# Optimization experiments

Hardware: AMD Instinct MI355X
Metric: run time of the kernel (lower is better)

## Reference

```python
import jax, jax.numpy as jnp
import numpy as np

STRIDE = 1
PADDING = 1
GROUPS = 1


def setup_inputs() -> dict:
    key = jax.random.key(0)
    kx, kw, kb = jax.random.split(key, 3)
    x_int = jax.random.randint(kx, (16, 256, 56, 56), 0, 127, dtype=jnp.int32)
    weight_int = jax.random.randint(kw, (256, 256, 3, 3), 0, 127, dtype=jnp.int32)
    bias_int = jax.random.randint(kb, (256,), 0, 127, dtype=jnp.int32)
    return {"x_int": x_int, "weight_int": weight_int, "bias_int": bias_int}


def reference(x_int, weight_int, bias_int):
    # Integer conv2d with int32 accumulation, exactly F.conv2d semantics.
    y = jax.lax.conv_general_dilated(
        x_int,
        weight_int,
        window_strides=(STRIDE, STRIDE),
        padding=((PADDING, PADDING), (PADDING, PADDING)),
        dimension_numbers=("NCHW", "OIHW", "NCHW"),
        feature_group_count=GROUPS,
    )
    # bias broadcast over [B, Cout, H, W]
    return y + bias_int[None, :, None, None]
```

## Files before the change

kernel.cpp:

```cpp
#include <hip/hip_runtime.h>


typedef int v4i  __attribute__((ext_vector_type(4)));
typedef int v16i __attribute__((ext_vector_type(16)));

#define X8_ROWSTRIDE 1856
#define X8_IMGSTRIDE 107648
#define X8_BYTES     13778944
#define W8_CHUNK     18432
#define XS_OFF       36864
#define XS_BUF       30720

typedef const __attribute__((address_space(1))) unsigned char* gptr_t;
typedef __attribute__((address_space(3))) unsigned char* lptr_t;

__device__ __forceinline__ int pack4(const int* p, int stride) {
  return (p[0] & 255) | ((p[stride] & 255) << 8) |
         ((p[2 * stride] & 255) << 16) | ((p[3 * stride] & 255) << 24);
}

__global__ __launch_bounds__(256)
void pack_all(const int* __restrict__ x, const int* __restrict__ wgt,
              unsigned char* __restrict__ ws8) {
  const int blk = blockIdx.x;
  if (blk < 784) {
    const int gid = blk * 256 + threadIdx.x;
    const int srcg = gid & 1;
    int t = gid >> 1;
    const int sq = t % 14;  t /= 14;
    const int row = t % 56 + 1;
    const int cb  = t / 56;
    const int chunk = cb >> 4, b = cb & 15;
    const int ci0 = chunk * 32 + srcg * 16;
    const int* src = x + (b * 256 + ci0) * 3136 + (row - 1) * 56 + 4 * sq;
    v4i L[16];
    #pragma unroll
    for (int ch = 0; ch < 16; ++ch) L[ch] = *(const v4i*)(src + ch * 3136);
    unsigned char* dstrow = ws8 + cb * X8_IMGSTRIDE + row * X8_ROWSTRIDE;
    #pragma unroll
    for (int j = 0; j < 4; ++j) {
      const int slot = 4 * sq + 1 + j;
      v4i g;
      #pragma unroll
      for (int d = 0; d < 4; ++d)
        g[d] = (L[4 * d][j] & 255) | ((L[4 * d + 1][j] & 255) << 8) |
               ((L[4 * d + 2][j] & 255) << 16) | ((L[4 * d + 3][j] & 255) << 24);
      const int p = (srcg + slot) & 1;
      *(v4i*)(dstrow + slot * 32 + p * 16) = g;
    }
  } else if (blk < 1012) {
    const int g2 = (blk - 784) * 256 + threadIdx.x;
    const int cb = g2 / 456;
    const int r  = g2 - cb * 456;
    int off;
    if (r < 232) {
      const int row = r < 116 ? 0 : 57;
      const int rr = r % 116;
      off = row * X8_ROWSTRIDE + (rr >> 1) * 32 + (rr & 1) * 16;
    } else {
      const int r2 = r - 232;
      const int row = (r2 >> 2) + 1;
      const int slot = (r2 & 2) ? 57 : 0;
      off = row * X8_ROWSTRIDE + slot * 32 + (r2 & 1) * 16;
    }
    *(v4i*)(ws8 + cb * X8_IMGSTRIDE + off) = (v4i){0, 0, 0, 0};
  } else {
    const int gw = (blk - 1012) * 256 + threadIdx.x;
    const int p = gw & 1;
    int t = gw >> 1;
    const int tap = t % 9;  t /= 9;
    const int co = t & 63;
    const int tcc = t >> 6;
    const int chunk = tcc & 7, cotile = tcc >> 3;
    const int srcg = (p + co) & 1;
    const int ci0 = chunk * 32 + srcg * 16;
    const int* src = wgt + ((cotile * 64 + co) * 256 + ci0) * 9 + tap;
    v4i v = (v4i){pack4(src, 9), pack4(src + 36, 9),
                  pack4(src + 72, 9), pack4(src + 108, 9)};
    *(v4i*)(ws8 + X8_BYTES + (t * 9 + tap) * 32 + p * 16) = v;
  }
}

__device__ __forceinline__ void stage_chunk(const unsigned char* wg,
                                            const unsigned char* xg,
                                            unsigned char* ldsb, int c, int tid) {
  const unsigned char* wsrc = wg + c * W8_CHUNK;
  unsigned char* wdst = ldsb + (c & 1) * W8_CHUNK;
  __builtin_amdgcn_global_load_lds((gptr_t)(wsrc + tid * 16),
                                   (lptr_t)(wdst + tid * 16), 16, 0, 0);
  __builtin_amdgcn_global_load_lds((gptr_t)(wsrc + 8192 + tid * 16),
                                   (lptr_t)(wdst + 8192 + tid * 16), 16, 0, 0);
  if (tid < 128)
    __builtin_amdgcn_global_load_lds((gptr_t)(wsrc + 16384 + tid * 16),
                                     (lptr_t)(wdst + 16384 + tid * 16), 16, 0, 0);
  const unsigned char* xsrc = xg + c * (16 * X8_IMGSTRIDE);
  unsigned char* xdst = ldsb + XS_OFF + (c & 1) * XS_BUF;
  #pragma unroll
  for (int i = 0; i < 3; ++i)
    __builtin_amdgcn_global_load_lds((gptr_t)(xsrc + i * 8192 + tid * 16),
                                     (lptr_t)(xdst + i * 8192 + tid * 16), 16, 0, 0);
  if (tid < 384)
    __builtin_amdgcn_global_load_lds((gptr_t)(xsrc + 24576 + tid * 16),
                                     (lptr_t)(xdst + 24576 + tid * 16), 16, 0, 0);
}

__global__ __launch_bounds__(512, 2)
void conv_main(const unsigned char* __restrict__ ws8, const int* __restrict__ bias,
               int* __restrict__ out) {
  __shared__ __align__(16) unsigned char lds[2 * W8_CHUNK + 2 * XS_BUF];
  __shared__ int bls[64];

  const int tid = threadIdx.x, lane = tid & 63, wv = tid >> 6;
  const int n = lane & 31, gq = lane >> 5;
  const int tc = blockIdx.y;
  const int hb = blockIdx.x;
  const int hg = hb >> 4, b = hb & 15;
  const int h0 = hg * 14;

  if (tid < 64) bls[tid] = bias[tc * 64 + tid];

  const int abase = n * 288 + (((gq + n) & 1) << 4);
  int boff[3][4];
  #pragma unroll
  for (int kw = 0; kw < 3; ++kw)
    #pragma unroll
    for (int bt = 0; bt < 4; ++bt) {
      int slot = bt * 16 + (n & 15) + kw;
      if (slot > 57) slot = 57;
      boff[kw][bt] = slot * 32 + (((gq + slot) & 1) << 4);
    }
  const int rbase = (2 * wv + (n >> 4)) * X8_ROWSTRIDE;

  v16i acc[2][4];
  #pragma unroll
  for (int i = 0; i < 2; ++i)
    #pragma unroll
    for (int j = 0; j < 4; ++j)
      acc[i][j] = (v16i){0,0,0,0,0,0,0,0,0,0,0,0,0,0,0,0};

  const unsigned char* wg = ws8 + X8_BYTES + tc * (8 * W8_CHUNK);
  const unsigned char* xg = ws8 + b * X8_IMGSTRIDE + h0 * X8_ROWSTRIDE;

  stage_chunk(wg, xg, lds, 0, tid);
  for (int c = 0; c < 8; ++c) {
    __syncthreads();
    if (c < 7) stage_chunk(wg, xg, lds, c + 1, tid);
    if (wv < 7) {
      const unsigned char* wls = lds + (c & 1) * W8_CHUNK;
      const unsigned char* xs  = lds + XS_OFF + (c & 1) * XS_BUF;
      #pragma unroll
      for (int kh = 0; kh < 3; ++kh) {
        const unsigned char* xr = xs + rbase + kh * X8_ROWSTRIDE;
        #pragma unroll
        for (int kw = 0; kw < 3; ++kw) {
          const int tap = kh * 3 + kw;
          const v4i a0 = *(const v4i*)(wls + abase + tap * 32);
          const v4i a1 = *(const v4i*)(wls + 9216 + abase + tap * 32);
          #pragma unroll
          for (int bt = 0; bt < 4; ++bt) {
            const v4i bb = *(const v4i*)(xr + boff[kw][bt]);
            acc[0][bt] = __builtin_amdgcn_mfma_i32_32x32x32_i8(a0, bb, acc[0][bt], 0, 0, 0);
            acc[1][bt] = __builtin_amdgcn_mfma_i32_32x32x32_i8(a1, bb, acc[1][bt], 0, 0, 0);
          }
        }
      }
    }
  }

  if (wv >= 7) return;
  const int h = h0 + 2 * wv + (n >> 4);
  const int wbase = lane & 15;
  #pragma unroll
  for (int ct = 0; ct < 2; ++ct) {
    #pragma unroll
    for (int r = 0; r < 16; ++r) {
      const int co64 = ct * 32 + (r & 3) + 8 * (r >> 2) + 4 * gq;
      const int bv = bls[co64];
      int* orow = out + ((b * 256 + tc * 64 + co64) * 56 + h) * 56;
      #pragma unroll
      for (int bt = 0; bt < 4; ++bt) {
        const int w0 = bt * 16 + wbase;
        if (w0 < 56) orow[w0] = acc[ct][bt][r] + bv;
      }
    }
  }
}

extern "C" void kernel_launch(void* const* d_in, const int* in_sizes, int n_in,
                              void* d_out, int out_size, void* d_ws, size_t ws_size,
                              hipStream_t stream) {
  const int* x    = (const int*)d_in[0];
  const int* w    = (const int*)d_in[1];
  const int* bias = (const int*)d_in[2];
  unsigned char* ws8 = (unsigned char*)d_ws;
  hipLaunchKernelGGL(pack_all, dim3(1156), dim3(256), 0, stream, x, w, ws8);
  hipLaunchKernelGGL(conv_main, dim3(64, 4, 1), dim3(512), 0, stream,
                     ws8, bias, (int*)d_out);
}
```

Measured before the change: 131.3 us.

## Triple-buffer LDS staging with vmcnt-gated barriers to prefetch two chunks ahead

Moves the weight and input staging in LDS from double to triple buffering, so chunk c+2 is prefetched while chunk c is computed. Each wait now uses s_waitcnt vmcnt(6) on only the older stage's async global-to-LDS loads, followed by a raw s_barrier, in place of a full __syncthreads. The per-thread load distribution is rebalanced so every thread issues exactly six loads per stage, which the vmcnt count relies on. The cost is LDS growing to about 147KB, which likely allows only one 512-thread block per CU. With a 256-block grid this may not reduce effective occupancy.

```diff
diff --git a/kernel.cpp b/kernel.cpp
--- a/kernel.cpp
+++ b/kernel.cpp
@@ -8,7 +8,7 @@
 #define X8_IMGSTRIDE 107648
 #define X8_BYTES     13778944
 #define W8_CHUNK     18432
-#define XS_OFF       36864
+#define XS_OFF       55296
 #define XS_BUF       30720
 
 typedef const __attribute__((address_space(1))) unsigned char* gptr_t;
@@ -83,31 +83,35 @@
 
 __device__ __forceinline__ void stage_chunk(const unsigned char* wg,
                                             const unsigned char* xg,
-                                            unsigned char* ldsb, int c, int tid) {
+                                            unsigned char* ldsb, int c, int buf,
+                                            int tid) {
   const unsigned char* wsrc = wg + c * W8_CHUNK;
-  unsigned char* wdst = ldsb + (c & 1) * W8_CHUNK;
-  __builtin_amdgcn_global_load_lds((gptr_t)(wsrc + tid * 16),
-                                   (lptr_t)(wdst + tid * 16), 16, 0, 0);
-  __builtin_amdgcn_global_load_lds((gptr_t)(wsrc + 8192 + tid * 16),
-                                   (lptr_t)(wdst + 8192 + tid * 16), 16, 0, 0);
-  if (tid < 128)
-    __builtin_amdgcn_global_load_lds((gptr_t)(wsrc + 16384 + tid * 16),
-                                     (lptr_t)(wdst + 16384 + tid * 16), 16, 0, 0);
   const unsigned char* xsrc = xg + c * (16 * X8_IMGSTRIDE);
-  unsigned char* xdst = ldsb + XS_OFF + (c & 1) * XS_BUF;
-  #pragma unroll
-  for (int i = 0; i < 3; ++i)
-    __builtin_amdgcn_global_load_lds((gptr_t)(xsrc + i * 8192 + tid * 16),
-                                     (lptr_t)(xdst + i * 8192 + tid * 16), 16, 0, 0);
-  if (tid < 384)
-    __builtin_amdgcn_global_load_lds((gptr_t)(xsrc + 24576 + tid * 16),
-                                     (lptr_t)(xdst + 24576 + tid * 16), 16, 0, 0);
+  unsigned char* wdst = ldsb + buf * W8_CHUNK;
+  unsigned char* xdst = ldsb + XS_OFF + buf * XS_BUF;
+  #pragma unroll
+  for (int i = 0; i < 2; ++i) {
+    const int o = (tid + i * 512) * 16;
+    __builtin_amdgcn_global_load_lds((gptr_t)(wsrc + o), (lptr_t)(wdst + o), 16, 0, 0);
+  }
+  if (tid < 128) {
+    const int o = (1024 + tid) * 16;
+    __builtin_amdgcn_global_load_lds((gptr_t)(wsrc + o), (lptr_t)(wdst + o), 16, 0, 0);
+  } else {
+    const int o = (tid - 128) * 16;
+    __builtin_amdgcn_global_load_lds((gptr_t)(xsrc + o), (lptr_t)(xdst + o), 16, 0, 0);
+  }
+  #pragma unroll
+  for (int i = 0; i < 3; ++i) {
+    const int o = (384 + tid + i * 512) * 16;
+    __builtin_amdgcn_global_load_lds((gptr_t)(xsrc + o), (lptr_t)(xdst + o), 16, 0, 0);
+  }
 }
 
 __global__ __launch_bounds__(512, 2)
 void conv_main(const unsigned char* __restrict__ ws8, const int* __restrict__ bias,
                int* __restrict__ out) {
-  __shared__ __align__(16) unsigned char lds[2 * W8_CHUNK + 2 * XS_BUF];
+  __shared__ __align__(16) unsigned char lds[3 * W8_CHUNK + 3 * XS_BUF];
   __shared__ int bls[64];
 
   const int tid = threadIdx.x, lane = tid & 63, wv = tid >> 6;
@@ -117,7 +121,10 @@
   const int hg = hb >> 4, b = hb & 15;
   const int h0 = hg * 14;
 
-  if (tid < 64) bls[tid] = bias[tc * 64 + tid];
+  if (tid < 64) {
+    bls[tid] = bias[tc * 64 + tid];
+    asm volatile("s_waitcnt lgkmcnt(0)" ::: "memory");
+  }
 
   const int abase = n * 288 + (((gq + n) & 1) << 4);
   int boff[3][4];
@@ -141,13 +148,18 @@
   const unsigned char* wg = ws8 + X8_BYTES + tc * (8 * W8_CHUNK);
   const unsigned char* xg = ws8 + b * X8_IMGSTRIDE + h0 * X8_ROWSTRIDE;
 
-  stage_chunk(wg, xg, lds, 0, tid);
+  stage_chunk(wg, xg, lds, 0, 0, tid);
+  stage_chunk(wg, xg, lds, 1, 1, tid);
+  int buf = 0, nbuf = 2;
   for (int c = 0; c < 8; ++c) {
-    __syncthreads();
-    if (c < 7) stage_chunk(wg, xg, lds, c + 1, tid);
+    if (c < 7) asm volatile("s_waitcnt vmcnt(6)" ::: "memory");
+    else       asm volatile("s_waitcnt vmcnt(0)" ::: "memory");
+    __builtin_amdgcn_s_barrier();
+    asm volatile("" ::: "memory");
+    if (c < 6) stage_chunk(wg, xg, lds, c + 2, nbuf, tid);
     if (wv < 7) {
-      const unsigned char* wls = lds + (c & 1) * W8_CHUNK;
-      const unsigned char* xs  = lds + XS_OFF + (c & 1) * XS_BUF;
+      const unsigned char* wls = lds + buf * W8_CHUNK;
+      const unsigned char* xs  = lds + XS_OFF + buf * XS_BUF;
       #pragma unroll
       for (int kh = 0; kh < 3; ++kh) {
         const unsigned char* xr = xs + rbase + kh * X8_ROWSTRIDE;
@@ -165,6 +177,8 @@
         }
       }
     }
+    buf  = (buf  == 2) ? 0 : buf  + 1;
+    nbuf = (nbuf == 2) ? 0 : nbuf + 1;
   }
 
   if (wv >= 7) return;
```

Result: no change. 132.9 us (+1.2%).
